# Optimization experiments

Measured on AMD Instinct MI355X. Metric: run time of the kernel, lower is better.

## Reference

```python
import jax, jax.numpy as jnp
import numpy as np

B, N, DIM = 2, 2048, 512
HEADS, DIM_HEAD = 8, 64
INNER = HEADS * DIM_HEAD  # 512
SCALE = DIM_HEAD ** -0.5


def setup_inputs() -> dict:
    key = jax.random.key(0)
    k1, k2, k3, k4, k5 = jax.random.split(key, 5)
    s = 0.02
    return {
        "x1": jax.random.normal(k1, (B, N, DIM), jnp.float32),
        "x2": jax.random.normal(k2, (B, N, DIM), jnp.float32),
        "W_qk": jax.random.normal(k3, (DIM, 2 * INNER), jnp.float32) * s,
        "W_v": jax.random.normal(k4, (DIM, INNER), jnp.float32) * s,
        "W_out": jax.random.normal(k5, (INNER, DIM), jnp.float32) * s,
        "b_out": jnp.zeros((DIM,), jnp.float32),
    }


def _split_heads(t):
    # [b, n, h*d] -> [b, h, n, d]
    b, n, _ = t.shape
    return t.reshape(b, n, HEADS, DIM_HEAD).transpose(0, 2, 1, 3)


def reference(x1, x2, W_qk, W_v, W_out, b_out):
    # to_qk(x1) -> chunk into k, v ; to_v(x2) -> q  (names in orig are swapped)
    kv = x1 @ W_qk                      # [b, n1, 2*inner]
    k, v = jnp.split(kv, 2, axis=-1)
    q = x2 @ W_v                        # [b, n2, inner]
    q, k, v = _split_heads(q), _split_heads(k), _split_heads(v)  # [b,h,n,d]
    dots = jnp.einsum("bhid,bhjd->bhij", q, k) * SCALE  # [b,h,n2,n1]
    attn = jax.nn.softmax(dots, axis=-1)
    out = jnp.einsum("bhij,bhjd->bhid", attn, v)         # [b,h,n2,d]
    out = out.transpose(0, 2, 1, 3).reshape(out.shape[0], out.shape[2], INNER)
    return out @ W_out + b_out          # [b, n2, dim]
```

## Files before the change

kernel.cpp:

```cpp
#include <hip/hip_runtime.h>

typedef short bf16x8 __attribute__((ext_vector_type(8)));
typedef short bf16x4 __attribute__((ext_vector_type(4)));
typedef float f32x4 __attribute__((ext_vector_type(4)));
typedef float f32x16 __attribute__((ext_vector_type(16)));
typedef unsigned short u16;
typedef u16 u16x8 __attribute__((ext_vector_type(8)));
typedef u16 u16x4 __attribute__((ext_vector_type(4)));

#define DEV __device__ __forceinline__

DEV u16 f2bf(float f) {
  unsigned u = __float_as_uint(f);
  u += 0x7fff + ((u >> 16) & 1);
  return (u16)(u >> 16);
}

DEV int pkbf(float lo, float hi) {
  return __builtin_amdgcn_perm(__float_as_uint(hi) + 0x8000u,
                               __float_as_uint(lo) + 0x8000u, 0x07060302u);
}

#define MFMA16(a, b, c) __builtin_amdgcn_mfma_f32_16x16x32_bf16(a, b, c, 0, 0, 0)
#define MFMA3216(a, b, c) __builtin_amdgcn_mfma_f32_32x32x16_bf16(a, b, c, 0, 0, 0)

#if __has_builtin(__builtin_amdgcn_mfma_f32_32x32x8bf16_1k)
#define HAVE_PV8 1
#define PVMFMA(a, b, c) __builtin_amdgcn_mfma_f32_32x32x8bf16_1k(a, b, c, 0, 0, 0)
#else
#define HAVE_PV8 0
#endif

__global__ __launch_bounds__(256) void wprep(
    const float* __restrict__ Wqk, const float* __restrict__ Wv,
    const float* __restrict__ Wout,
    u16* __restrict__ WqkT, u16* __restrict__ WvT, u16* __restrict__ WoutT) {
  __shared__ float tf[32][33];
  int bx = blockIdx.x, t = threadIdx.x;
  const float* src; u16* dst; int Ncols; int id;
  if (bx < 512)      { id = bx;       src = Wqk;  dst = WqkT;  Ncols = 1024; }
  else if (bx < 768) { id = bx - 512; src = Wv;   dst = WvT;   Ncols = 512; }
  else               { id = bx - 768; src = Wout; dst = WoutT; Ncols = 512; }
  int tilesPerRow = Ncols >> 5;
  int tr = id / tilesPerRow, tc = id % tilesPerRow;
  int r0 = tr * 32, c0 = tc * 32;
  {
    int r = t >> 3, c4 = (t & 7) * 4;
    float4 v = *(const float4*)(src + (long)(r0 + r) * Ncols + c0 + c4);
    tf[r][c4] = v.x; tf[r][c4 + 1] = v.y; tf[r][c4 + 2] = v.z; tf[r][c4 + 3] = v.w;
  }
  __syncthreads();
  {
    int c = t >> 3, r4 = (t & 7) * 4;
    u16x4 o;
    o[0] = f2bf(tf[r4][c]); o[1] = f2bf(tf[r4 + 1][c]);
    o[2] = f2bf(tf[r4 + 2][c]); o[3] = f2bf(tf[r4 + 3][c]);
    *(u16x4*)(dst + (long)(c0 + c) * 512 + r0 + r4) = o;
  }
}

__global__ __launch_bounds__(256) void qkv_gemm(
    const float* __restrict__ x1, const float* __restrict__ x2,
    const u16* __restrict__ WqkT, const u16* __restrict__ WvT,
    u16* __restrict__ out_q, u16* __restrict__ out_k, u16* __restrict__ out_vt) {
  __shared__ u16 sA[2][128 * 40];
  __shared__ u16 sB[2][64 * 40];
  int bx = blockIdx.x, t = threadIdx.x;
  bool isQ = bx < 256;
  int bx2 = isQ ? bx : bx - 256;
  const float* Ap = isQ ? x2 : x1;
  const u16* BT = isQ ? WvT : WqkT;
  int m0 = (bx2 & 31) * 128, n0 = (bx2 >> 5) * 64;
  int w = t >> 6, l = t & 63, lm = l & 15, lq = l >> 4;

  f32x4 zero = {0.f, 0.f, 0.f, 0.f};
  f32x4 acc[2][4];
#pragma unroll
  for (int i = 0; i < 2; ++i)
#pragma unroll
    for (int j = 0; j < 4; ++j) acc[i][j] = zero;

  int sm = t >> 2;
  int skc = (t & 3) * 8;
  const float* gAf = Ap + (long)(m0 + sm) * 512 + skc;
  const u16* gB = BT + (long)(n0 + sm) * 512 + skc;

  auto loadA = [&](int kt, int rows) {
    long off = (long)rows * 512 + kt * 32;
    float4 f0 = *(const float4*)(gAf + off);
    float4 f1 = *(const float4*)(gAf + off + 4);
    bf16x8 o;
    o[0] = (short)f2bf(f0.x); o[1] = (short)f2bf(f0.y);
    o[2] = (short)f2bf(f0.z); o[3] = (short)f2bf(f0.w);
    o[4] = (short)f2bf(f1.x); o[5] = (short)f2bf(f1.y);
    o[6] = (short)f2bf(f1.z); o[7] = (short)f2bf(f1.w);
    return o;
  };

  bf16x8 a0 = loadA(0, 0);
  bf16x8 a1 = loadA(0, 64);
  bf16x8 b0 = *(const bf16x8*)(gB);
  *(bf16x8*)(sA[0] + sm * 40 + skc) = a0;
  *(bf16x8*)(sA[0] + (sm + 64) * 40 + skc) = a1;
  *(bf16x8*)(sB[0] + sm * 40 + skc) = b0;
  __syncthreads();

  for (int kt = 0; kt < 16; ++kt) {
    int cur = kt & 1;
    if (kt < 15) {
      a0 = loadA(kt + 1, 0);
      a1 = loadA(kt + 1, 64);
      b0 = *(const bf16x8*)(gB + (kt + 1) * 32);
    }
    bf16x8 af[2], bfr[4];
    af[0] = *(const bf16x8*)(sA[cur] + (w * 32 + lm) * 40 + lq * 8);
    af[1] = *(const bf16x8*)(sA[cur] + (w * 32 + 16 + lm) * 40 + lq * 8);
#pragma unroll
    for (int s = 0; s < 4; ++s)
      bfr[s] = *(const bf16x8*)(sB[cur] + (s * 16 + lm) * 40 + lq * 8);
#pragma unroll
    for (int ms = 0; ms < 2; ++ms)
#pragma unroll
      for (int s = 0; s < 4; ++s)
        acc[ms][s] = MFMA16(af[ms], bfr[s], acc[ms][s]);
    if (kt < 15) {
      int nxt = 1 - cur;
      *(bf16x8*)(sA[nxt] + sm * 40 + skc) = a0;
      *(bf16x8*)(sA[nxt] + (sm + 64) * 40 + skc) = a1;
      *(bf16x8*)(sB[nxt] + sm * 40 + skc) = b0;
    }
    __syncthreads();
  }

#pragma unroll
  for (int ms = 0; ms < 2; ++ms) {
    int gmBase = m0 + w * 32 + ms * 16 + lq * 4;
#pragma unroll
    for (int s = 0; s < 4; ++s) {
      int gc = n0 + s * 16 + lm;
      int b = gmBase >> 11, n = gmBase & 2047;
      if (isQ) {
#pragma unroll
        for (int r = 0; r < 4; ++r)
          out_q[(((long)(b << 3) + (gc >> 6)) * 2048 + n + r) * 64 + (gc & 63)] =
              f2bf(acc[ms][s][r] * 0.125f);
      } else if (gc < 512) {
#pragma unroll
        for (int r = 0; r < 4; ++r)
          out_k[(((long)(b << 3) + (gc >> 6)) * 2048 + n + r) * 64 + (gc & 63)] =
              f2bf(acc[ms][s][r]);
      } else {
        int c = gc - 512, h = c >> 6, d = c & 63;
        u16x4 vv;
#pragma unroll
        for (int r = 0; r < 4; ++r) vv[r] = f2bf(acc[ms][s][r]);
        *(u16x4*)(out_vt + (((long)(b << 3) + h) * 64 + d) * 2048 + n) = vv;
      }
    }
  }
}

__global__ __launch_bounds__(256, 2) void attn(
    const u16* __restrict__ Q, const u16* __restrict__ K,
    const u16* __restrict__ Vt, u16* __restrict__ O) {
  int id = blockIdx.x;
  int bh = id & 15, qt = id >> 4;
  int b = bh >> 3, h = bh & 7;
  const u16* Kh = K + (long)bh * 2048 * 64;
  const u16* Vh = Vt + (long)bh * 64 * 2048;
  int t = threadIdx.x, w = t >> 6, lane = t & 63, ln = lane & 31, hi = lane >> 5;
  int g = w & 1, kh = w >> 1;

  __shared__ u16 sK[2][2][64 * 72];
  __shared__ u16 sV[2][2][64 * 72];

  bf16x8 qf[4];
  {
    const u16* qp = Q + (long)bh * 2048 * 64 + (long)(qt * 64 + g * 32 + ln) * 64 + hi * 8;
#pragma unroll
    for (int dc = 0; dc < 4; ++dc) qf[dc] = *(const bf16x8*)(qp + dc * 16);
  }

  f32x16 accOa[2], accOb[2];
#pragma unroll
  for (int dt = 0; dt < 2; ++dt)
#pragma unroll
    for (int i = 0; i < 16; ++i) { accOa[dt][i] = 0.f; accOb[dt][i] = 0.f; }
  float dacc = 0.f;

  int tp = t & 127;
  int r = tp >> 1, half = tp & 1;
  const u16* gK = Kh + (long)(kh * 1024 + r) * 64 + half * 32;
  const u16* gV = Vh + (long)r * 2048 + kh * 1024 + half * 32;
  int woff = r * 72 + half * 32;

  bf16x8 kp[4], vp[4];
#pragma unroll
  for (int i = 0; i < 4; ++i) {
    kp[i] = *(const bf16x8*)(gK + i * 8);
    vp[i] = *(const bf16x8*)(gV + i * 8);
  }
#pragma unroll
  for (int i = 0; i < 4; ++i) {
    *(bf16x8*)(sK[kh][0] + woff + i * 8) = kp[i];
    *(bf16x8*)(sV[kh][0] + woff + i * 8) = vp[i];
  }
  __syncthreads();

  for (int jt = 0; jt < 16; ++jt) {
    int cur = jt & 1;
    if (jt < 15) {
      long ko = (long)(jt + 1) * 64 * 64, vo = (long)(jt + 1) * 64;
#pragma unroll
      for (int i = 0; i < 4; ++i) {
        kp[i] = *(const bf16x8*)(gK + ko + i * 8);
        vp[i] = *(const bf16x8*)(gV + vo + i * 8);
      }
    }
    const u16* bK = sK[kh][cur];
    const u16* bV = sV[kh][cur];

#pragma unroll
    for (int kt2 = 0; kt2 < 2; ++kt2) {
      f32x16 st1, st2;
#pragma unroll
      for (int i = 0; i < 16; ++i) { st1[i] = 0.f; st2[i] = 0.f; }
      bf16x8 kf0 = *(const bf16x8*)(bK + (kt2 * 32 + ln) * 72 + 0 * 16 + hi * 8);
      bf16x8 kf1 = *(const bf16x8*)(bK + (kt2 * 32 + ln) * 72 + 1 * 16 + hi * 8);
      bf16x8 kf2 = *(const bf16x8*)(bK + (kt2 * 32 + ln) * 72 + 2 * 16 + hi * 8);
      bf16x8 kf3 = *(const bf16x8*)(bK + (kt2 * 32 + ln) * 72 + 3 * 16 + hi * 8);
      st1 = MFMA3216(kf0, qf[0], st1);
      st2 = MFMA3216(kf1, qf[1], st2);
      st1 = MFMA3216(kf2, qf[2], st1);
      st2 = MFMA3216(kf3, qf[3], st2);
      float p[16];
#pragma unroll
      for (int i = 0; i < 16; ++i) {
        float e = __expf(st1[i] + st2[i]);
        p[i] = e;
        dacc += e;
      }
#if HAVE_PV8
#pragma unroll
      for (int c = 0; c < 4; ++c) {
        union { int2 i2; bf16x4 v; } u;
        u.i2.x = pkbf(p[c * 4 + 0], p[c * 4 + 1]);
        u.i2.y = pkbf(p[c * 4 + 2], p[c * 4 + 3]);
#pragma unroll
        for (int dt = 0; dt < 2; ++dt) {
          bf16x4 vf = *(const bf16x4*)(bV + (dt * 32 + ln) * 72 + kt2 * 32 + c * 8 + hi * 4);
          if (c & 1)
            accOb[dt] = PVMFMA(vf, u.v, accOb[dt]);
          else
            accOa[dt] = PVMFMA(vf, u.v, accOa[dt]);
        }
      }
#else
#pragma unroll
      for (int c2 = 0; c2 < 2; ++c2) {
        int o0x = pkbf(p[c2 * 8 + 0], p[c2 * 8 + 1]);
        int o0y = pkbf(p[c2 * 8 + 2], p[c2 * 8 + 3]);
        int o1x = pkbf(p[c2 * 8 + 4], p[c2 * 8 + 5]);
        int o1y = pkbf(p[c2 * 8 + 6], p[c2 * 8 + 7]);
        int s0x = __shfl_xor(o0x, 32), s0y = __shfl_xor(o0y, 32);
        int s1x = __shfl_xor(o1x, 32), s1y = __shfl_xor(o1y, 32);
        union { int4 i4; bf16x8 v; } u;
        if (hi) { u.i4.x = s1x; u.i4.y = s1y; u.i4.z = o1x; u.i4.w = o1y; }
        else    { u.i4.x = o0x; u.i4.y = o0y; u.i4.z = s0x; u.i4.w = s0y; }
#pragma unroll
        for (int dt = 0; dt < 2; ++dt) {
          bf16x8 vf = *(const bf16x8*)(bV + (dt * 32 + ln) * 72 + kt2 * 32 + c2 * 16 + hi * 8);
          if (c2 & 1)
            accOb[dt] = MFMA3216(vf, u.v, accOb[dt]);
          else
            accOa[dt] = MFMA3216(vf, u.v, accOa[dt]);
        }
      }
#endif
    }

    if (jt < 15) {
      int nxt = cur ^ 1;
#pragma unroll
      for (int i = 0; i < 4; ++i) {
        *(bf16x8*)(sK[kh][nxt] + woff + i * 8) = kp[i];
        *(bf16x8*)(sV[kh][nxt] + woff + i * 8) = vp[i];
      }
    }
    __syncthreads();
  }

  f32x16 accO[2];
#pragma unroll
  for (int dt = 0; dt < 2; ++dt)
#pragma unroll
    for (int i = 0; i < 16; ++i) accO[dt][i] = accOa[dt][i] + accOb[dt][i];

  float* cb = (float*)&sK[0][0][0];
  float* base = cb + g * 4224;
  if (kh == 1) {
#pragma unroll
    for (int dt = 0; dt < 2; ++dt)
#pragma unroll
      for (int i = 0; i < 16; ++i)
        base[(dt * 16 + i) * 64 + hi * 32 + ln] = accO[dt][i];
    base[4096 + hi * 32 + ln] = dacc;
  }
  __syncthreads();
  if (kh == 0) {
#pragma unroll
    for (int dt = 0; dt < 2; ++dt)
#pragma unroll
      for (int i = 0; i < 16; ++i)
        accO[dt][i] += base[(dt * 16 + i) * 64 + hi * 32 + ln];
    dacc += base[4096 + hi * 32 + ln];
    dacc += __shfl_xor(dacc, 32);
    float inv = 1.f / dacc;

    u16* Ob = O + ((long)b * 2048 + qt * 64 + g * 32 + ln) * 512 + h * 64;
#pragma unroll
    for (int dt = 0; dt < 2; ++dt)
#pragma unroll
      for (int gq = 0; gq < 4; ++gq) {
        u16x4 o;
#pragma unroll
        for (int rr = 0; rr < 4; ++rr) o[rr] = f2bf(accO[dt][gq * 4 + rr] * inv);
        *(u16x4*)(Ob + dt * 32 + gq * 8 + hi * 4) = o;
      }
  }
}

__global__ __launch_bounds__(128) void out_gemm(
    const u16* __restrict__ A, const u16* __restrict__ BT,
    float* __restrict__ out_f, const float* __restrict__ bias) {
  __shared__ u16 sA[2][64 * 40];
  __shared__ u16 sB[2][32 * 40];
  int t = threadIdx.x, bx = blockIdx.x;
  int m0 = (bx & 63) * 64, n0 = (bx >> 6) * 32;
  int w = t >> 6, l = t & 63, lm = l & 15, lq = l >> 4;

  f32x4 zero = {0.f, 0.f, 0.f, 0.f};
  f32x4 acc[2][2];
#pragma unroll
  for (int i = 0; i < 2; ++i)
#pragma unroll
    for (int j = 0; j < 2; ++j) acc[i][j] = zero;

  int ar = t >> 1, akc = (t & 1) * 16;
  int br = t >> 2, bkc = (t & 3) * 8;
  const u16* gA = A + (long)(m0 + ar) * 512 + akc;
  const u16* gB = BT + (long)(n0 + br) * 512 + bkc;

  bf16x8 a0 = *(const bf16x8*)(gA);
  bf16x8 a1 = *(const bf16x8*)(gA + 8);
  bf16x8 b0 = *(const bf16x8*)(gB);
  *(bf16x8*)(sA[0] + ar * 40 + akc) = a0;
  *(bf16x8*)(sA[0] + ar * 40 + akc + 8) = a1;
  *(bf16x8*)(sB[0] + br * 40 + bkc) = b0;
  __syncthreads();

  for (int kt = 0; kt < 16; ++kt) {
    int cur = kt & 1;
    if (kt < 15) {
      a0 = *(const bf16x8*)(gA + (kt + 1) * 32);
      a1 = *(const bf16x8*)(gA + (kt + 1) * 32 + 8);
      b0 = *(const bf16x8*)(gB + (kt + 1) * 32);
    }
    bf16x8 af[2], bfr[2];
    af[0] = *(const bf16x8*)(sA[cur] + (w * 32 + lm) * 40 + lq * 8);
    af[1] = *(const bf16x8*)(sA[cur] + (w * 32 + 16 + lm) * 40 + lq * 8);
    bfr[0] = *(const bf16x8*)(sB[cur] + (lm)*40 + lq * 8);
    bfr[1] = *(const bf16x8*)(sB[cur] + (16 + lm) * 40 + lq * 8);
#pragma unroll
    for (int ms = 0; ms < 2; ++ms)
#pragma unroll
      for (int s = 0; s < 2; ++s)
        acc[ms][s] = MFMA16(af[ms], bfr[s], acc[ms][s]);
    if (kt < 15) {
      int nxt = 1 - cur;
      *(bf16x8*)(sA[nxt] + ar * 40 + akc) = a0;
      *(bf16x8*)(sA[nxt] + ar * 40 + akc + 8) = a1;
      *(bf16x8*)(sB[nxt] + br * 40 + bkc) = b0;
    }
    __syncthreads();
  }

#pragma unroll
  for (int ms = 0; ms < 2; ++ms) {
    int gmBase = m0 + w * 32 + ms * 16 + lq * 4;
#pragma unroll
    for (int s = 0; s < 2; ++s) {
      int gc = n0 + s * 16 + lm;
      float bv = bias[gc];
#pragma unroll
      for (int r = 0; r < 4; ++r)
        out_f[(long)(gmBase + r) * 512 + gc] = acc[ms][s][r] + bv;
    }
  }
}

extern "C" void kernel_launch(void* const* d_in, const int* in_sizes, int n_in,
                              void* d_out, int out_size, void* d_ws, size_t ws_size,
                              hipStream_t stream) {
  const float* x1 = (const float*)d_in[0];
  const float* x2 = (const float*)d_in[1];
  const float* Wqk = (const float*)d_in[2];
  const float* Wv = (const float*)d_in[3];
  const float* Wout = (const float*)d_in[4];
  const float* bout = (const float*)d_in[5];
  float* out = (float*)d_out;

  u16* ws = (u16*)d_ws;
  const long SZ = 2097152;
  u16* Qw = ws;
  u16* Kw = ws + SZ;
  u16* Vtw = ws + 2 * SZ;
  u16* Ow = ws + 3 * SZ;
  u16* WqkT = ws + 4 * SZ;
  u16* WvT = WqkT + 524288;
  u16* WoutT = WvT + 262144;

  wprep<<<1024, 256, 0, stream>>>(Wqk, Wv, Wout, WqkT, WvT, WoutT);
  qkv_gemm<<<768, 256, 0, stream>>>(x1, x2, WqkT, WvT, Qw, Kw, Vtw);
  attn<<<512, 256, 0, stream>>>(Qw, Kw, Vtw, Ow);
  out_gemm<<<1024, 128, 0, stream>>>(Ow, WoutT, out, bout);
}
```

Baseline: 129.8 us.

## Stage attention K/V via direct global-to-LDS loads with XOR swizzle and exp2

K and V tiles now go straight from global memory into LDS using global_load_lds. The padded layout is replaced by an XOR-swizzled one, and the double buffer becomes a single 32KB buffer. The smaller LDS footprint allows launch bounds of 4 blocks per CU, which is meant to hide load latency through occupancy rather than through in-block prefetch. The softmax scale now folds log2(e) into Q so a raw exp2 can replace __expf, and the two split output accumulators are merged into one. The tradeoff is that each tile load sits between two barriers with no overlap inside the block, and the merged accumulators lengthen the MFMA dependency chain.

```diff
diff --git a/kernel.cpp b/kernel.cpp
--- a/kernel.cpp
+++ b/kernel.cpp
@@ -5,6 +5,7 @@
 typedef float f32x4 __attribute__((ext_vector_type(4)));
 typedef float f32x16 __attribute__((ext_vector_type(16)));
 typedef unsigned short u16;
+typedef unsigned int u32;
 typedef u16 u16x8 __attribute__((ext_vector_type(8)));
 typedef u16 u16x4 __attribute__((ext_vector_type(4)));
 
@@ -30,6 +31,19 @@
 #else
 #define HAVE_PV8 0
 #endif
+
+#if __has_builtin(__builtin_amdgcn_exp2f)
+#define QSCALE 0.18033688011112042f
+#define EXPFN(x) __builtin_amdgcn_exp2f(x)
+#else
+#define QSCALE 0.125f
+#define EXPFN(x) __expf(x)
+#endif
+
+#define GLD16(gp, lp)                                                     \
+  __builtin_amdgcn_global_load_lds(                                       \
+      (const __attribute__((address_space(1))) u32*)(gp),                 \
+      (__attribute__((address_space(3))) u32*)(lp), 16, 0, 0)
 
 __global__ __launch_bounds__(256) void wprep(
     const float* __restrict__ Wqk, const float* __restrict__ Wv,
@@ -143,7 +157,7 @@
 #pragma unroll
         for (int r = 0; r < 4; ++r)
           out_q[(((long)(b << 3) + (gc >> 6)) * 2048 + n + r) * 64 + (gc & 63)] =
-              f2bf(acc[ms][s][r] * 0.125f);
+              f2bf(acc[ms][s][r] * QSCALE);
       } else if (gc < 512) {
 #pragma unroll
         for (int r = 0; r < 4; ++r)
@@ -160,7 +174,7 @@
   }
 }
 
-__global__ __launch_bounds__(256, 2) void attn(
+__global__ __launch_bounds__(256, 4) void attn(
     const u16* __restrict__ Q, const u16* __restrict__ K,
     const u16* __restrict__ Vt, u16* __restrict__ O) {
   int id = blockIdx.x;
@@ -171,8 +185,9 @@
   int t = threadIdx.x, w = t >> 6, lane = t & 63, ln = lane & 31, hi = lane >> 5;
   int g = w & 1, kh = w >> 1;
 
-  __shared__ u16 sK[2][2][64 * 72];
-  __shared__ u16 sV[2][2][64 * 72];
+  __shared__ u16 smem[2][2][4096];
+  u16* sKh = smem[0][kh];
+  u16* sVh = smem[1][kh];
 
   bf16x8 qf[4];
   {
@@ -181,54 +196,43 @@
     for (int dc = 0; dc < 4; ++dc) qf[dc] = *(const bf16x8*)(qp + dc * 16);
   }
 
-  f32x16 accOa[2], accOb[2];
+  f32x16 accO[2];
 #pragma unroll
   for (int dt = 0; dt < 2; ++dt)
 #pragma unroll
-    for (int i = 0; i < 16; ++i) { accOa[dt][i] = 0.f; accOb[dt][i] = 0.f; }
+    for (int i = 0; i < 16; ++i) accO[dt][i] = 0.f;
   float dacc = 0.f;
 
-  int tp = t & 127;
-  int r = tp >> 1, half = tp & 1;
-  const u16* gK = Kh + (long)(kh * 1024 + r) * 64 + half * 32;
-  const u16* gV = Vh + (long)r * 2048 + kh * 1024 + half * 32;
-  int woff = r * 72 + half * 32;
-
-  bf16x8 kp[4], vp[4];
-#pragma unroll
-  for (int i = 0; i < 4; ++i) {
-    kp[i] = *(const bf16x8*)(gK + i * 8);
-    vp[i] = *(const bf16x8*)(gV + i * 8);
-  }
-#pragma unroll
-  for (int i = 0; i < 4; ++i) {
-    *(bf16x8*)(sK[kh][0] + woff + i * 8) = kp[i];
-    *(bf16x8*)(sV[kh][0] + woff + i * 8) = vp[i];
-  }
+  int lrow = lane >> 3;
+  int swz = ((lane & 7) ^ lrow) * 8;
+  const u16* gKl = Kh + (long)(kh * 1024 + g * 32 + lrow) * 64 + swz;
+  const u16* gVl = Vh + (long)(g * 32 + lrow) * 2048 + kh * 1024 + swz;
+
+  auto stage = [&](int jt) {
+    const u16* gk = gKl + (long)jt * 4096;
+    const u16* gv = gVl + jt * 64;
+#pragma unroll
+    for (int i = 0; i < 4; ++i) {
+      GLD16(gk + i * 512, sKh + (g * 32 + i * 8) * 64);
+      GLD16(gv + (long)i * 16384, sVh + (g * 32 + i * 8) * 64);
+    }
+  };
+
+  stage(0);
   __syncthreads();
 
+  int swl = ln & 7;
   for (int jt = 0; jt < 16; ++jt) {
-    int cur = jt & 1;
-    if (jt < 15) {
-      long ko = (long)(jt + 1) * 64 * 64, vo = (long)(jt + 1) * 64;
-#pragma unroll
-      for (int i = 0; i < 4; ++i) {
-        kp[i] = *(const bf16x8*)(gK + ko + i * 8);
-        vp[i] = *(const bf16x8*)(gV + vo + i * 8);
-      }
-    }
-    const u16* bK = sK[kh][cur];
-    const u16* bV = sV[kh][cur];
-
 #pragma unroll
     for (int kt2 = 0; kt2 < 2; ++kt2) {
+      int rowK = (kt2 * 32 + ln) * 64;
       f32x16 st1, st2;
 #pragma unroll
       for (int i = 0; i < 16; ++i) { st1[i] = 0.f; st2[i] = 0.f; }
-      bf16x8 kf0 = *(const bf16x8*)(bK + (kt2 * 32 + ln) * 72 + 0 * 16 + hi * 8);
-      bf16x8 kf1 = *(const bf16x8*)(bK + (kt2 * 32 + ln) * 72 + 1 * 16 + hi * 8);
-      bf16x8 kf2 = *(const bf16x8*)(bK + (kt2 * 32 + ln) * 72 + 2 * 16 + hi * 8);
-      bf16x8 kf3 = *(const bf16x8*)(bK + (kt2 * 32 + ln) * 72 + 3 * 16 + hi * 8);
+      bf16x8 kf0 = *(const bf16x8*)(sKh + rowK + ((0 * 2 + hi) ^ swl) * 8);
+      bf16x8 kf1 = *(const bf16x8*)(sKh + rowK + ((1 * 2 + hi) ^ swl) * 8);
+      bf16x8 kf2 = *(const bf16x8*)(sKh + rowK + ((2 * 2 + hi) ^ swl) * 8);
+      bf16x8 kf3 = *(const bf16x8*)(sKh + rowK + ((3 * 2 + hi) ^ swl) * 8);
       st1 = MFMA3216(kf0, qf[0], st1);
       st2 = MFMA3216(kf1, qf[1], st2);
       st1 = MFMA3216(kf2, qf[2], st1);
@@ -236,7 +240,7 @@
       float p[16];
 #pragma unroll
       for (int i = 0; i < 16; ++i) {
-        float e = __expf(st1[i] + st2[i]);
+        float e = EXPFN(st1[i] + st2[i]);
         p[i] = e;
         dacc += e;
       }
@@ -248,11 +252,9 @@
         u.i2.y = pkbf(p[c * 4 + 2], p[c * 4 + 3]);
 #pragma unroll
         for (int dt = 0; dt < 2; ++dt) {
-          bf16x4 vf = *(const bf16x4*)(bV + (dt * 32 + ln) * 72 + kt2 * 32 + c * 8 + hi * 4);
-          if (c & 1)
-            accOb[dt] = PVMFMA(vf, u.v, accOb[dt]);
-          else
-            accOa[dt] = PVMFMA(vf, u.v, accOa[dt]);
+          bf16x4 vf = *(const bf16x4*)(sVh + (dt * 32 + ln) * 64 +
+                                       (((kt2 * 4 + c) ^ swl) * 8) + hi * 4);
+          accO[dt] = PVMFMA(vf, u.v, accO[dt]);
         }
       }
 #else
@@ -269,42 +271,29 @@
         else    { u.i4.x = o0x; u.i4.y = o0y; u.i4.z = s0x; u.i4.w = s0y; }
 #pragma unroll
         for (int dt = 0; dt < 2; ++dt) {
-          bf16x8 vf = *(const bf16x8*)(bV + (dt * 32 + ln) * 72 + kt2 * 32 + c2 * 16 + hi * 8);
-          if (c2 & 1)
-            accOb[dt] = MFMA3216(vf, u.v, accOb[dt]);
-          else
-            accOa[dt] = MFMA3216(vf, u.v, accOa[dt]);
+          bf16x8 vf = *(const bf16x8*)(sVh + (dt * 32 + ln) * 64 +
+                                       (((kt2 * 4 + c2 * 2 + hi) ^ swl) * 8));
+          accO[dt] = MFMA3216(vf, u.v, accO[dt]);
         }
       }
 #endif
     }
-
+    __syncthreads();
     if (jt < 15) {
-      int nxt = cur ^ 1;
-#pragma unroll
-      for (int i = 0; i < 4; ++i) {
-        *(bf16x8*)(sK[kh][nxt] + woff + i * 8) = kp[i];
-        *(bf16x8*)(sV[kh][nxt] + woff + i * 8) = vp[i];
-      }
-    }
-    __syncthreads();
-  }
-
-  f32x16 accO[2];
-#pragma unroll
-  for (int dt = 0; dt < 2; ++dt)
-#pragma unroll
-    for (int i = 0; i < 16; ++i) accO[dt][i] = accOa[dt][i] + accOb[dt][i];
-
-  float* cb = (float*)&sK[0][0][0];
-  float* base = cb + g * 4224;
+      stage(jt + 1);
+      __syncthreads();
+    }
+  }
+
+  float* cb = (float*)&smem[0][0][0];
+  float* base = cb + g * 2112;
   if (kh == 1) {
 #pragma unroll
     for (int dt = 0; dt < 2; ++dt)
 #pragma unroll
       for (int i = 0; i < 16; ++i)
         base[(dt * 16 + i) * 64 + hi * 32 + ln] = accO[dt][i];
-    base[4096 + hi * 32 + ln] = dacc;
+    base[2048 + hi * 32 + ln] = dacc;
   }
   __syncthreads();
   if (kh == 0) {
@@ -313,7 +302,7 @@
 #pragma unroll
       for (int i = 0; i < 16; ++i)
         accO[dt][i] += base[(dt * 16 + i) * 64 + hi * 32 + ln];
-    dacc += base[4096 + hi * 32 + ln];
+    dacc += base[2048 + hi * 32 + ln];
     dacc += __shfl_xor(dacc, 32);
     float inv = 1.f / dacc;
 
```

After: 128.4 us, median of 2. No clear change (-1.1%).
